# Optimization experiments

Hardware: AMD Instinct MI355X
Metric: run time of the kernel (lower is better)

The kernel has to match this reference:

```python
import jax, jax.numpy as jnp
import numpy as np

ALPHA = 0.2        # LeakyReLU negative slope
NEG_INF = -9e15    # mask value used by the torch module


def setup_inputs() -> dict:
    key = jax.random.key(0)
    ks = jax.random.split(key, 7)
    B, T, N, Cin = 4, 12, 1024, 64
    Fout, Em = 64, 16
    x = jax.random.normal(ks[0], (B, T, N, Cin), dtype=jnp.float32)
    adj = jax.random.randint(ks[1], (N, N), 0, 2, dtype=jnp.int32)
    emb1 = jax.random.normal(ks[2], (N, Em), dtype=jnp.float32)
    emb2 = jax.random.normal(ks[3], (N, Em), dtype=jnp.float32)
    W = jax.random.normal(ks[4], (Cin, Fout), dtype=jnp.float32) * (1.0 / np.sqrt(Cin))
    a = jax.random.normal(ks[5], (2 * Fout, 1), dtype=jnp.float32) * 0.1
    a2 = jax.random.normal(ks[6], (2 * Em, 1), dtype=jnp.float32) * 0.1
    return {"x": x, "adj": adj, "emb1": emb1, "emb2": emb2, "W": W, "a": a, "a2": a2}


def reference(x, adj, emb1, emb2, W, a, a2):
    B, T, N, Cin = x.shape
    Fout = W.shape[1]
    Em = emb1.shape[1]
    # Linear projection, fold batch*time: Wh [BT, N, Fout]
    Wh = jnp.einsum('btnc,cf->btnf', x, W).reshape(B * T, N, Fout)
    # Additive attention scores from node features
    s1 = Wh @ a[:Fout, 0]          # [BT, N]
    s2 = Wh @ a[Fout:, 0]          # [BT, N]
    e1 = s1[:, :, None] + s2[:, None, :]   # [BT, N, N]
    # Additive scores from static embeddings (shared across batch*time)
    f1 = emb1 @ a2[:Em, 0]         # [N]
    f2 = emb2 @ a2[Em:, 0]         # [N]
    e2 = f1[:, None] + f2[None, :]          # [N, N]
    e = jax.nn.leaky_relu(e1 + e2[None, :, :], negative_slope=ALPHA)
    # Adjacency mask + row softmax (dropout is inference no-op)
    att = jnp.where(adj[None, :, :] > 0, e, jnp.float32(NEG_INF))
    att = jax.nn.softmax(att, axis=-1)
    h_prime = att @ Wh                       # [BT, N, Fout]
    return jax.nn.elu(h_prime.reshape(B, T, N, Fout))
```

## Files before the change

### kernel.cpp

```cpp
#include <hip/hip_runtime.h>
#include <hip/hip_bf16.h>
#include <math.h>

#define BT 48
#define N 1024
#define F 64
#define CIN 64
#define EM 16
#define LRELU_A 0.2f

typedef short bf16x8 __attribute__((ext_vector_type(8)));
typedef float f32x4  __attribute__((ext_vector_type(4)));

__device__ __forceinline__ unsigned short f2bf(float f) {
    unsigned int u = __float_as_uint(f);
    return (unsigned short)((u + 0x7FFFu + ((u >> 16) & 1u)) >> 16);
}

__global__ __launch_bounds__(256) void k_proj_misc(
    const float* __restrict__ x, const float* __restrict__ W,
    const float* __restrict__ a,
    const int* __restrict__ adj,
    const float* __restrict__ emb1, const float* __restrict__ emb2,
    const float* __restrict__ a2,
    unsigned short* __restrict__ WhSw,
    float* __restrict__ s1, float* __restrict__ s2,
    unsigned int* __restrict__ adjBits,
    float* __restrict__ f1, float* __restrict__ f2)
{
    const int tid = threadIdx.x;
    const int b   = blockIdx.x;

    if (b >= 768) {
        if (b < 896) {
            const int idx = (b - 768) * 256 + tid;
            const int r = idx >> 5, w32 = idx & 31;
            const int* p = adj + (size_t)r * N + w32 * 32;
            unsigned int m = 0;
#pragma unroll
            for (int j = 0; j < 32; ++j) m |= (p[j] > 0 ? 1u : 0u) << j;
            adjBits[idx] = m;
        } else {
            const int n = (b - 896) * 256 + tid;
            if (n < N) {
                float v1 = 0.f, v2 = 0.f;
#pragma unroll
                for (int k = 0; k < EM; ++k) {
                    v1 = fmaf(emb1[n * EM + k], a2[k], v1);
                    v2 = fmaf(emb2[n * EM + k], a2[EM + k], v2);
                }
                f1[n] = v1; f2[n] = v2;
            }
        }
        return;
    }

    __shared__ __align__(16) float sx[64 * 64];
    __shared__ __align__(16) float sWT[64 * 68];
    __shared__ __align__(16) unsigned short sT[64 * 80];

    const int bt  = b >> 4;
    const int n0  = (b & 15) * 64;
    const size_t grow = (size_t)bt * N + n0;

    {
        const float4* xv = (const float4*)(x + grow * CIN);
        float4* sxv = (float4*)sx;
        for (int i = tid; i < 64 * CIN / 4; i += 256) sxv[i] = xv[i];
        for (int i = tid; i < CIN * F; i += 256)
            sWT[(i & 63) * 68 + (i >> 6)] = W[i];
    }
    __syncthreads();

    const int f = tid & 63;
    const int w = tid >> 6;
    const float a1 = a[f], a2c = a[F + f];

    float acc[16];
#pragma unroll
    for (int t = 0; t < 16; ++t) acc[t] = 0.f;

    for (int cb = 0; cb < CIN; cb += 4) {
        const float4 wv = *(const float4*)&sWT[f * 68 + cb];
#pragma unroll
        for (int t = 0; t < 16; ++t) {
            const float4 xv = *(const float4*)&sx[(w * 16 + t) * 64 + cb];
            acc[t] = fmaf(xv.x, wv.x, acc[t]);
            acc[t] = fmaf(xv.y, wv.y, acc[t]);
            acc[t] = fmaf(xv.z, wv.z, acc[t]);
            acc[t] = fmaf(xv.w, wv.w, acc[t]);
        }
    }

#pragma unroll
    for (int t = 0; t < 16; ++t) {
        float v1 = acc[t] * a1;
        float v2 = acc[t] * a2c;
#pragma unroll
        for (int off = 32; off >= 1; off >>= 1) {
            v1 += __shfl_xor(v1, off, 64);
            v2 += __shfl_xor(v2, off, 64);
        }
        if (f == 0) {
            s1[grow + w * 16 + t] = v1;
            s2[grow + w * 16 + t] = v2;
        }
        sT[f * 80 + w * 16 + t] = f2bf(acc[t]);
    }
    __syncthreads();

    {
        const int ff = tid >> 2, q = tid & 3;
        const int nb0 = (b & 15) * 2;
#pragma unroll
        for (int nbL = 0; nbL < 2; ++nbL) {
            const size_t dst = ((size_t)(bt * 32 + nb0 + nbL) * 64 + ff) * 32 + q * 8;
            *(uint4*)&WhSw[dst] = *(const uint4*)&sT[ff * 80 + nbL * 32 + q * 8];
        }
    }
}

__global__ __launch_bounds__(256, 3) void k_attn(
    const unsigned int* __restrict__ adjBits,
    const unsigned short* __restrict__ WhSw,
    const float* __restrict__ s1, const float* __restrict__ s2,
    const float* __restrict__ f1v, const float* __restrict__ f2v,
    float* __restrict__ out)
{
    __shared__ __align__(16) float sC[N];
    __shared__ __align__(16) unsigned short sB[8192];

    const int tid  = threadIdx.x;
    const int xcd = blockIdx.x & 7;
    const int idx = blockIdx.x >> 3;
    const int bt  = xcd * 6 + (idx >> 4);
    const int i0  = (idx & 15) * 64;
    const int lane = tid & 63;
    const int w    = tid >> 6;
    const int q    = lane >> 4;
    const int m15  = lane & 15;

    for (int j = tid; j < N; j += 256) sC[j] = s2[bt * N + j] + f2v[j];
    __syncthreads();

    float mx = -1e30f;
#pragma unroll
    for (int t = 0; t < 4; ++t) {
        const float4 v = *(const float4*)&sC[t * 256 + lane * 4];
        mx = fmaxf(mx, fmaxf(fmaxf(v.x, v.y), fmaxf(v.z, v.w)));
    }
#pragma unroll
    for (int off = 32; off >= 1; off >>= 1) mx = fmaxf(mx, __shfl_xor(mx, off, 64));

    const int growq = i0 + w * 16 + m15;
    const float r   = s1[bt * N + growq] + f1v[growq];
    const float sm  = r + mx;
    const float mhat = (sm > 0.f) ? sm : LRELU_A * sm;
    float lsum = 0.f;

    const unsigned int* abRow = adjBits + growq * 32;
    const unsigned short* gBbt = WhSw + (size_t)bt * 65536;

    f32x4 acc[4];
#pragma unroll
    for (int ct = 0; ct < 4; ++ct)
#pragma unroll
        for (int e = 0; e < 4; ++e) acc[ct][e] = 0.f;

    for (int ch = 0; ch < 8; ++ch) {
        const int k0 = ch * 128;
        const unsigned short* gB = gBbt + ch * 8192;

        uint4 st[4];
#pragma unroll
        for (int k = 0; k < 4; ++k)
            st[k] = *(const uint4*)(gB + k * 2048 + tid * 8);

        const uint4 ab = *(const uint4*)&abRow[ch * 4];
        const unsigned int abw[4] = {ab.x, ab.y, ab.z, ab.w};

        bf16x8 afr[4];
#pragma unroll
        for (int ks = 0; ks < 4; ++ks) {
            const float4 c0 = *(const float4*)&sC[k0 + ks * 32 + q * 8];
            const float4 c1 = *(const float4*)&sC[k0 + ks * 32 + q * 8 + 4];
            const float cj[8] = {c0.x, c0.y, c0.z, c0.w, c1.x, c1.y, c1.z, c1.w};
            const unsigned int mb = (abw[ks] >> (q * 8)) & 0xFFu;
            union { unsigned int u[4]; bf16x8 v; } A;
#pragma unroll
            for (int jp = 0; jp < 4; ++jp) {
                const float s0 = r + cj[2 * jp];
                const float s1v = r + cj[2 * jp + 1];
                const float e0 = (s0 > 0.f) ? s0 : LRELU_A * s0;
                const float e1 = (s1v > 0.f) ? s1v : LRELU_A * s1v;
                float p0 = __expf(e0 - mhat);
                float p1 = __expf(e1 - mhat);
                p0 = ((mb >> (2 * jp)) & 1u) ? p0 : 0.f;
                p1 = ((mb >> (2 * jp + 1)) & 1u) ? p1 : 0.f;
                lsum += p0 + p1;
                A.u[jp] = __builtin_amdgcn_perm(
                    __float_as_uint(p1) + 0x8000u,
                    __float_as_uint(p0) + 0x8000u, 0x07060302u);
            }
            afr[ks] = A.v;
        }

#pragma unroll
        for (int k = 0; k < 4; ++k)
            *(uint4*)((char*)sB + k * 4096 + tid * 16) = st[k];
        __syncthreads();

#pragma unroll
        for (int ct = 0; ct < 4; ++ct) {
#pragma unroll
            for (int ks = 0; ks < 4; ++ks) {
                const bf16x8 bfr = *(const bf16x8*)
                    ((const char*)sB + ks * 4096 + (ct * 16 + m15) * 64 + q * 16);
                acc[ct] = __builtin_amdgcn_mfma_f32_16x16x32_bf16(
                    afr[ks], bfr, acc[ct], 0, 0, 0);
            }
        }
        __syncthreads();
    }

    lsum += __shfl_xor(lsum, 16, 64);
    lsum += __shfl_xor(lsum, 32, 64);

    float rinv[4];
#pragma unroll
    for (int reg = 0; reg < 4; ++reg)
        rinv[reg] = 1.f / __shfl(lsum, q * 4 + reg, 64);

#pragma unroll
    for (int ct = 0; ct < 4; ++ct) {
#pragma unroll
        for (int reg = 0; reg < 4; ++reg) {
            float h = acc[ct][reg] * rinv[reg];
            h = (h > 0.f) ? h : (__expf(h) - 1.f);
            out[(size_t)(bt * N + i0 + w * 16 + q * 4 + reg) * F + ct * 16 + m15] = h;
        }
    }
}

extern "C" void kernel_launch(void* const* d_in, const int* in_sizes, int n_in,
                              void* d_out, int out_size, void* d_ws, size_t ws_size,
                              hipStream_t stream)
{
    const float* x    = (const float*)d_in[0];
    const int*   adj  = (const int*)  d_in[1];
    const float* emb1 = (const float*)d_in[2];
    const float* emb2 = (const float*)d_in[3];
    const float* W    = (const float*)d_in[4];
    const float* a    = (const float*)d_in[5];
    const float* a2   = (const float*)d_in[6];
    float* out = (float*)d_out;

    unsigned short* WhSw = (unsigned short*)d_ws;
    float* s1 = (float*)(WhSw + (size_t)BT * 65536);
    float* s2 = s1 + BT * N;
    float* f1 = s2 + BT * N;
    float* f2 = f1 + N;
    unsigned int* adjBits = (unsigned int*)(f2 + N);

    hipLaunchKernelGGL(k_proj_misc, dim3(900), dim3(256), 0, stream,
                       x, W, a, adj, emb1, emb2, a2, WhSw, s1, s2, adjBits, f1, f2);
    hipLaunchKernelGGL(k_attn, dim3(BT * 16), dim3(256), 0, stream,
                       adjBits, WhSw, s1, s2, f1, f2, out);
}
```

Baseline: 124.1 us.

## Double-buffer Wh tiles in LDS and simplify LeakyReLU-exp math

The attention kernel now double-buffers the Wh chunk in shared memory. The global loads and the softmax-probability computation for the next chunk are issued around the MFMA work on the current chunk, so only one barrier per chunk remains. The LeakyReLU-minus-max is also rewritten as a max of two precomputed affine forms, and masked entries become -1e30 before exp instead of being selected afterwards. This doubles the sB LDS footprint and raises register pressure, since two A-fragment sets plus staged loads are live at once, which may hurt occupancy at the 3-blocks launch bound.

```diff
diff --git a/kernel.cpp b/kernel.cpp
--- a/kernel.cpp
+++ b/kernel.cpp
@@ -128,7 +128,7 @@
     float* __restrict__ out)
 {
     __shared__ __align__(16) float sC[N];
-    __shared__ __align__(16) unsigned short sB[8192];
+    __shared__ __align__(16) unsigned short sB[2][8192];
 
     const int tid  = threadIdx.x;
     const int xcd = blockIdx.x & 7;
@@ -153,9 +153,11 @@
     for (int off = 32; off >= 1; off >>= 1) mx = fmaxf(mx, __shfl_xor(mx, off, 64));
 
     const int growq = i0 + w * 16 + m15;
-    const float r   = s1[bt * N + growq] + f1v[growq];
-    const float sm  = r + mx;
-    const float mhat = (sm > 0.f) ? sm : LRELU_A * sm;
+    const float r    = s1[bt * N + growq] + f1v[growq];
+    const float smx  = r + mx;
+    const float mhat = fmaxf(smx, LRELU_A * smx);
+    const float A1 = r - mhat;
+    const float A2 = LRELU_A * r - mhat;
     float lsum = 0.f;
 
     const unsigned int* abRow = adjBits + growq * 32;
@@ -167,19 +169,16 @@
 #pragma unroll
         for (int e = 0; e < 4; ++e) acc[ct][e] = 0.f;
 
-    for (int ch = 0; ch < 8; ++ch) {
-        const int k0 = ch * 128;
+    auto stage_issue = [&](int ch, uint4* st) {
         const unsigned short* gB = gBbt + ch * 8192;
-
-        uint4 st[4];
 #pragma unroll
         for (int k = 0; k < 4; ++k)
             st[k] = *(const uint4*)(gB + k * 2048 + tid * 8);
-
+    };
+    auto make_afr = [&](int ch, bf16x8* afr) {
+        const int k0 = ch * 128;
         const uint4 ab = *(const uint4*)&abRow[ch * 4];
         const unsigned int abw[4] = {ab.x, ab.y, ab.z, ab.w};
-
-        bf16x8 afr[4];
 #pragma unroll
         for (int ks = 0; ks < 4; ++ks) {
             const float4 c0 = *(const float4*)&sC[k0 + ks * 32 + q * 8];
@@ -189,14 +188,12 @@
             union { unsigned int u[4]; bf16x8 v; } A;
 #pragma unroll
             for (int jp = 0; jp < 4; ++jp) {
-                const float s0 = r + cj[2 * jp];
-                const float s1v = r + cj[2 * jp + 1];
-                const float e0 = (s0 > 0.f) ? s0 : LRELU_A * s0;
-                const float e1 = (s1v > 0.f) ? s1v : LRELU_A * s1v;
-                float p0 = __expf(e0 - mhat);
-                float p1 = __expf(e1 - mhat);
-                p0 = ((mb >> (2 * jp)) & 1u) ? p0 : 0.f;
-                p1 = ((mb >> (2 * jp + 1)) & 1u) ? p1 : 0.f;
+                float t0 = fmaxf(A1 + cj[2 * jp],     fmaf(cj[2 * jp],     LRELU_A, A2));
+                float t1 = fmaxf(A1 + cj[2 * jp + 1], fmaf(cj[2 * jp + 1], LRELU_A, A2));
+                t0 = ((mb >> (2 * jp)) & 1u)     ? t0 : -1e30f;
+                t1 = ((mb >> (2 * jp + 1)) & 1u) ? t1 : -1e30f;
+                const float p0 = __expf(t0);
+                const float p1 = __expf(t1);
                 lsum += p0 + p1;
                 A.u[jp] = __builtin_amdgcn_perm(
                     __float_as_uint(p1) + 0x8000u,
@@ -204,21 +201,42 @@
             }
             afr[ks] = A.v;
         }
-
+    };
+    auto commit = [&](int ch, const uint4* st) {
+        char* dst = (char*)sB[ch & 1];
 #pragma unroll
         for (int k = 0; k < 4; ++k)
-            *(uint4*)((char*)sB + k * 4096 + tid * 16) = st[k];
-        __syncthreads();
-
-#pragma unroll
-        for (int ct = 0; ct < 4; ++ct) {
+            *(uint4*)(dst + k * 4096 + tid * 16) = st[k];
+    };
+    auto mfma_chunk = [&](int ch, const bf16x8* afr) {
+        const char* src = (const char*)sB[ch & 1];
+#pragma unroll
+        for (int ct = 0; ct < 4; ++ct)
 #pragma unroll
             for (int ks = 0; ks < 4; ++ks) {
-                const bf16x8 bfr = *(const bf16x8*)
-                    ((const char*)sB + ks * 4096 + (ct * 16 + m15) * 64 + q * 16);
+                const bf16x8 b = *(const bf16x8*)
+                    (src + ks * 4096 + (ct * 16 + m15) * 64 + q * 16);
                 acc[ct] = __builtin_amdgcn_mfma_f32_16x16x32_bf16(
-                    afr[ks], bfr, acc[ct], 0, 0, 0);
+                    afr[ks], b, acc[ct], 0, 0, 0);
             }
+    };
+
+    uint4 st[4];
+    bf16x8 afrA[4], afrB[4];
+
+    stage_issue(0, st);
+    make_afr(0, afrA);
+    commit(0, st);
+    __syncthreads();
+
+    for (int ch = 0; ch < 8; ++ch) {
+        bf16x8* cur = (ch & 1) ? afrB : afrA;
+        bf16x8* nxt = (ch & 1) ? afrA : afrB;
+        if (ch < 7) stage_issue(ch + 1, st);
+        mfma_chunk(ch, cur);
+        if (ch < 7) {
+            make_afr(ch + 1, nxt);
+            commit(ch + 1, st);
         }
         __syncthreads();
     }
```

Measured after the change: 131.2 us. 5.7% more time.
